# Optimization experiments

Measured on AMD Instinct MI355X. Metric: run time of the kernel, lower is better.

## Reference

```python
import jax, jax.numpy as jnp
import numpy as np

NCLASS = 21  # num_classes from init
EPS = 1e-6


def setup_inputs() -> dict:
    key = jax.random.key(0)
    k1, k2 = jax.random.split(key)
    feats = jax.random.normal(k1, (8, 256, 64, 64), dtype=jnp.float32)
    masks = jax.random.randint(k2, (8, 256, 256), 0, NCLASS, dtype=jnp.int32)
    return {"feats": feats, "masks": masks}


def reference(feats, masks):
    # feats: [B, C, h, w] float; masks: [B, H, W] int labels
    B, C, _, _ = feats.shape
    H, W = masks.shape[-2:]
    # F.interpolate(..., mode='bilinear', align_corners=False) == half-pixel bilinear resize
    f = jax.image.resize(feats, (B, C, H, W), method="bilinear")  # [B,C,H,W]
    f_flat = f.reshape(B, C, H * W)  # [B,C,P]

    # labels > nclass (e.g. 255 ignore) are clamped to the dump bucket `nclass`;
    # pixels with label == nclass are excluded (one_hot drops out-of-range rows).
    lbl = jnp.where(masks > NCLASS, NCLASS, masks).reshape(B, H * W)  # [B,P]
    onehot = jax.nn.one_hot(lbl, NCLASS, dtype=f.dtype)  # [B,P,K], dump bucket -> all zeros

    # segment-reduce: per-image per-class feature sums and pixel counts
    sums = jnp.einsum("bcp,bpk->bkc", f_flat, onehot)  # [B,K,C]
    counts = onehot.sum(axis=1)  # [B,K]
    per_img = sums / (counts[..., None] + EPS)  # [B,K,C]; absent classes -> ~0, matching torch loop skip
    prototypes = per_img.mean(axis=0)  # [K,C] (sum over batch / b)
    return prototypes
```

## Files before the change

### kernel.cpp

```cpp
#include <hip/hip_runtime.h>

#define NK 21
#define NC 256
#define NSRC 64
#define NOUT 256
#define NB 8
#define EPS 1e-6f

__device__ __forceinline__ void lds_fadd(float* p, float v) {
  __hip_atomic_fetch_add(p, v, __ATOMIC_RELAXED, __HIP_MEMORY_SCOPE_WORKGROUP);
}

__device__ __forceinline__ void glb_fadd(float* p, float v) {
  __hip_atomic_fetch_add(p, v, __ATOMIC_RELAXED, __HIP_MEMORY_SCOPE_AGENT);
}

__global__ __launch_bounds__(256, 4)
void proto_main(const float* __restrict__ feats,
                const int* __restrict__ masks,
                float* __restrict__ psum,
                float* __restrict__ pcnt) {
  __shared__ __align__(16) float Wl[NK * 32];
  __shared__ int hist[NK];

  const int tid = threadIdx.x;
  const int r0 = blockIdx.x;
  const int b = blockIdx.y;
  const int z = blockIdx.z;

  const float4* fbase = (const float4*)(
      feats + ((size_t)(b * NC + tid) << 12) + (size_t)r0 * 64 + 32 * z);
  const float4 f0 = fbase[0], f1 = fbase[1], f2 = fbase[2], f3 = fbase[3];
  const float4 f4 = fbase[4], f5 = fbase[5], f6 = fbase[6], f7 = fbase[7];

  for (int i = tid; i < NK * 32; i += 256) Wl[i] = 0.f;
  if (tid < NK) hist[tid] = 0;
  __syncthreads();

  int ylo = 4 * r0 - 2; if (ylo < 0) ylo = 0;
  int yhi = 4 * r0 + 5; if (yhi > NOUT - 1) yhi = NOUT - 1;
  const int xlo = z ? 126 : 0;
  const int npix = (yhi - ylo + 1) * 130;
  const int own_lo = 4 * r0;

  for (int i = tid; i < npix; i += 256) {
    const int x = xlo + i % 130;
    const int y = ylo + i / 130;
    const int lbl = masks[((size_t)b * NOUT + y) * NOUT + x];
    if ((unsigned)lbl < NK) {
      const int ry = y >> 2, py = y & 3;
      const int j0y = (py < 2) ? ry - 1 : ry;
      const float fy = (py == 0) ? 0.625f : (py == 1) ? 0.875f
                     : (py == 2) ? 0.125f : 0.375f;
      const int rx = x >> 2, px = x & 3;
      const int j0x = (px < 2) ? rx - 1 : rx;
      const float fx = (px == 0) ? 0.625f : (px == 1) ? 0.875f
                     : (px == 2) ? 0.125f : 0.375f;

      const int cx0 = (j0x < 0) ? 0 : j0x;
      const int cx1 = (j0x + 1 > NSRC - 1) ? NSRC - 1 : j0x + 1;
      const float wx0 = 1.f - fx, wx1 = fx;
      const int ry0 = (j0y < 0) ? 0 : j0y;
      const int ry1 = (j0y + 1 > NSRC - 1) ? NSRC - 1 : j0y + 1;
      const float wy0 = 1.f - fy, wy1 = fy;

      float* Wk = &Wl[lbl * 32];
      if (ry0 == r0) {
        if ((cx0 >> 5) == z) lds_fadd(&Wk[cx0 & 31], wy0 * wx0);
        if ((cx1 >> 5) == z) lds_fadd(&Wk[cx1 & 31], wy0 * wx1);
      }
      if (ry1 == r0) {
        if ((cx0 >> 5) == z) lds_fadd(&Wk[cx0 & 31], wy1 * wx0);
        if ((cx1 >> 5) == z) lds_fadd(&Wk[cx1 & 31], wy1 * wx1);
      }
      if (y >= own_lo && y < own_lo + 4 && (x >> 7) == z)
        atomicAdd(&hist[lbl], 1);
    }
  }
  __syncthreads();

  float acc[NK];
#pragma unroll
  for (int k = 0; k < NK; ++k) acc[k] = 0.f;

  const float4* wb = (const float4*)Wl;
#pragma unroll
  for (int k = 0; k < NK; ++k) {
    const float4 w0 = wb[k * 8 + 0], w1 = wb[k * 8 + 1];
    const float4 w2 = wb[k * 8 + 2], w3 = wb[k * 8 + 3];
    float a = acc[k];
    a = fmaf(f0.x, w0.x, a); a = fmaf(f0.y, w0.y, a);
    a = fmaf(f0.z, w0.z, a); a = fmaf(f0.w, w0.w, a);
    a = fmaf(f1.x, w1.x, a); a = fmaf(f1.y, w1.y, a);
    a = fmaf(f1.z, w1.z, a); a = fmaf(f1.w, w1.w, a);
    a = fmaf(f2.x, w2.x, a); a = fmaf(f2.y, w2.y, a);
    a = fmaf(f2.z, w2.z, a); a = fmaf(f2.w, w2.w, a);
    a = fmaf(f3.x, w3.x, a); a = fmaf(f3.y, w3.y, a);
    a = fmaf(f3.z, w3.z, a); a = fmaf(f3.w, w3.w, a);
    acc[k] = a;
  }
#pragma unroll
  for (int k = 0; k < NK; ++k) {
    const float4 w4 = wb[k * 8 + 4], w5 = wb[k * 8 + 5];
    const float4 w6 = wb[k * 8 + 6], w7 = wb[k * 8 + 7];
    float a = acc[k];
    a = fmaf(f4.x, w4.x, a); a = fmaf(f4.y, w4.y, a);
    a = fmaf(f4.z, w4.z, a); a = fmaf(f4.w, w4.w, a);
    a = fmaf(f5.x, w5.x, a); a = fmaf(f5.y, w5.y, a);
    a = fmaf(f5.z, w5.z, a); a = fmaf(f5.w, w5.w, a);
    a = fmaf(f6.x, w6.x, a); a = fmaf(f6.y, w6.y, a);
    a = fmaf(f6.z, w6.z, a); a = fmaf(f6.w, w6.w, a);
    a = fmaf(f7.x, w7.x, a); a = fmaf(f7.y, w7.y, a);
    a = fmaf(f7.z, w7.z, a); a = fmaf(f7.w, w7.w, a);
    acc[k] = a;
  }

#pragma unroll
  for (int k = 0; k < NK; ++k)
    glb_fadd(&psum[((size_t)b * NK + k) * NC + tid], acc[k]);
  if (tid < NK) glb_fadd(&pcnt[(size_t)b * NK + tid], (float)hist[tid]);
}

__global__ __launch_bounds__(256)
void proto_final(const float* __restrict__ psum,
                 const float* __restrict__ pcnt,
                 float* __restrict__ out) {
  const int k = blockIdx.x;
  const int c = threadIdx.x;
  float a = 0.f;
#pragma unroll
  for (int b = 0; b < NB; ++b)
    a += psum[((size_t)b * NK + k) * NC + c] / (pcnt[(size_t)b * NK + k] + EPS);
  out[(size_t)k * NC + c] = a * 0.125f;
}

extern "C" void kernel_launch(void* const* d_in, const int* in_sizes, int n_in,
                              void* d_out, int out_size, void* d_ws, size_t ws_size,
                              hipStream_t stream) {
  const float* feats = (const float*)d_in[0];
  const int* masks = (const int*)d_in[1];
  float* out = (float*)d_out;

  float* psum = (float*)d_ws;
  float* pcnt = psum + (size_t)NB * NK * NC;
  const size_t zbytes = ((size_t)NB * NK * NC + (size_t)NB * NK) * 4;

  hipMemsetAsync(d_ws, 0, zbytes, stream);
  proto_main<<<dim3(64, NB, 2), 256, 0, stream>>>(feats, masks, psum, pcnt);
  proto_final<<<dim3(NK), 256, 0, stream>>>(psum, pcnt, out);
}
```

Baseline: 110.6 us.

## Replace global atomics with per-slice partial buffers and drop memset

New measurement: 102.9 us. 1.08x faster.

```diff
diff --git a/kernel.cpp b/kernel.cpp
--- a/kernel.cpp
+++ b/kernel.cpp
@@ -5,21 +5,22 @@
 #define NSRC 64
 #define NOUT 256
 #define NB 8
+#define NSL 128
 #define EPS 1e-6f
 
 __device__ __forceinline__ void lds_fadd(float* p, float v) {
   __hip_atomic_fetch_add(p, v, __ATOMIC_RELAXED, __HIP_MEMORY_SCOPE_WORKGROUP);
 }
-
 __device__ __forceinline__ void glb_fadd(float* p, float v) {
   __hip_atomic_fetch_add(p, v, __ATOMIC_RELAXED, __HIP_MEMORY_SCOPE_AGENT);
 }
 
-__global__ __launch_bounds__(256, 4)
+__global__ __launch_bounds__(128, 4)
 void proto_main(const float* __restrict__ feats,
                 const int* __restrict__ masks,
                 float* __restrict__ psum,
-                float* __restrict__ pcnt) {
+                float* __restrict__ pcnt,
+                float* __restrict__ out) {
   __shared__ __align__(16) float Wl[NK * 32];
   __shared__ int hist[NK];
 
@@ -28,12 +29,19 @@
   const int b = blockIdx.y;
   const int z = blockIdx.z;
 
-  const float4* fbase = (const float4*)(
+  const float4* fb0 = (const float4*)(
       feats + ((size_t)(b * NC + tid) << 12) + (size_t)r0 * 64 + 32 * z);
-  const float4 f0 = fbase[0], f1 = fbase[1], f2 = fbase[2], f3 = fbase[3];
-  const float4 f4 = fbase[4], f5 = fbase[5], f6 = fbase[6], f7 = fbase[7];
+  const float4* fb1 = (const float4*)(
+      feats + ((size_t)(b * NC + tid + 128) << 12) + (size_t)r0 * 64 + 32 * z);
+  const float4 f0 = fb0[0], f1 = fb0[1], f2 = fb0[2], f3 = fb0[3];
+  const float4 f4 = fb0[4], f5 = fb0[5], f6 = fb0[6], f7 = fb0[7];
+  const float4 g0 = fb1[0], g1 = fb1[1], g2 = fb1[2], g3 = fb1[3];
+  const float4 g4 = fb1[4], g5 = fb1[5], g6 = fb1[6], g7 = fb1[7];
 
-  for (int i = tid; i < NK * 32; i += 256) Wl[i] = 0.f;
+  if (r0 == 0 && b == 0 && z == 0)
+    for (int i = tid; i < NK * NC; i += 128) out[i] = 0.f;
+
+  for (int i = tid; i < NK * 32; i += 128) Wl[i] = 0.f;
   if (tid < NK) hist[tid] = 0;
   __syncthreads();
 
@@ -43,7 +51,7 @@
   const int npix = (yhi - ylo + 1) * 130;
   const int own_lo = 4 * r0;
 
-  for (int i = tid; i < npix; i += 256) {
+  for (int i = tid; i < npix; i += 128) {
     const int x = xlo + i % 130;
     const int y = ylo + i / 130;
     const int lbl = masks[((size_t)b * NOUT + y) * NOUT + x];
@@ -79,46 +87,52 @@
   }
   __syncthreads();
 
-  float acc[NK];
-#pragma unroll
-  for (int k = 0; k < NK; ++k) acc[k] = 0.f;
-
+  const int sl = r0 * 2 + z;
+  float* dst = psum + ((size_t)(b * NSL + sl) * NK) * NC;
   const float4* wb = (const float4*)Wl;
 #pragma unroll
   for (int k = 0; k < NK; ++k) {
     const float4 w0 = wb[k * 8 + 0], w1 = wb[k * 8 + 1];
     const float4 w2 = wb[k * 8 + 2], w3 = wb[k * 8 + 3];
-    float a = acc[k];
-    a = fmaf(f0.x, w0.x, a); a = fmaf(f0.y, w0.y, a);
-    a = fmaf(f0.z, w0.z, a); a = fmaf(f0.w, w0.w, a);
-    a = fmaf(f1.x, w1.x, a); a = fmaf(f1.y, w1.y, a);
-    a = fmaf(f1.z, w1.z, a); a = fmaf(f1.w, w1.w, a);
-    a = fmaf(f2.x, w2.x, a); a = fmaf(f2.y, w2.y, a);
-    a = fmaf(f2.z, w2.z, a); a = fmaf(f2.w, w2.w, a);
-    a = fmaf(f3.x, w3.x, a); a = fmaf(f3.y, w3.y, a);
-    a = fmaf(f3.z, w3.z, a); a = fmaf(f3.w, w3.w, a);
-    acc[k] = a;
-  }
-#pragma unroll
-  for (int k = 0; k < NK; ++k) {
     const float4 w4 = wb[k * 8 + 4], w5 = wb[k * 8 + 5];
     const float4 w6 = wb[k * 8 + 6], w7 = wb[k * 8 + 7];
-    float a = acc[k];
-    a = fmaf(f4.x, w4.x, a); a = fmaf(f4.y, w4.y, a);
-    a = fmaf(f4.z, w4.z, a); a = fmaf(f4.w, w4.w, a);
-    a = fmaf(f5.x, w5.x, a); a = fmaf(f5.y, w5.y, a);
-    a = fmaf(f5.z, w5.z, a); a = fmaf(f5.w, w5.w, a);
-    a = fmaf(f6.x, w6.x, a); a = fmaf(f6.y, w6.y, a);
-    a = fmaf(f6.z, w6.z, a); a = fmaf(f6.w, w6.w, a);
-    a = fmaf(f7.x, w7.x, a); a = fmaf(f7.y, w7.y, a);
-    a = fmaf(f7.z, w7.z, a); a = fmaf(f7.w, w7.w, a);
-    acc[k] = a;
+    float a0 = 0.f, a1 = 0.f;
+    a0 = fmaf(f0.x, w0.x, a0); a0 = fmaf(f0.y, w0.y, a0);
+    a0 = fmaf(f0.z, w0.z, a0); a0 = fmaf(f0.w, w0.w, a0);
+    a0 = fmaf(f1.x, w1.x, a0); a0 = fmaf(f1.y, w1.y, a0);
+    a0 = fmaf(f1.z, w1.z, a0); a0 = fmaf(f1.w, w1.w, a0);
+    a0 = fmaf(f2.x, w2.x, a0); a0 = fmaf(f2.y, w2.y, a0);
+    a0 = fmaf(f2.z, w2.z, a0); a0 = fmaf(f2.w, w2.w, a0);
+    a0 = fmaf(f3.x, w3.x, a0); a0 = fmaf(f3.y, w3.y, a0);
+    a0 = fmaf(f3.z, w3.z, a0); a0 = fmaf(f3.w, w3.w, a0);
+    a0 = fmaf(f4.x, w4.x, a0); a0 = fmaf(f4.y, w4.y, a0);
+    a0 = fmaf(f4.z, w4.z, a0); a0 = fmaf(f4.w, w4.w, a0);
+    a0 = fmaf(f5.x, w5.x, a0); a0 = fmaf(f5.y, w5.y, a0);
+    a0 = fmaf(f5.z, w5.z, a0); a0 = fmaf(f5.w, w5.w, a0);
+    a0 = fmaf(f6.x, w6.x, a0); a0 = fmaf(f6.y, w6.y, a0);
+    a0 = fmaf(f6.z, w6.z, a0); a0 = fmaf(f6.w, w6.w, a0);
+    a0 = fmaf(f7.x, w7.x, a0); a0 = fmaf(f7.y, w7.y, a0);
+    a0 = fmaf(f7.z, w7.z, a0); a0 = fmaf(f7.w, w7.w, a0);
+    a1 = fmaf(g0.x, w0.x, a1); a1 = fmaf(g0.y, w0.y, a1);
+    a1 = fmaf(g0.z, w0.z, a1); a1 = fmaf(g0.w, w0.w, a1);
+    a1 = fmaf(g1.x, w1.x, a1); a1 = fmaf(g1.y, w1.y, a1);
+    a1 = fmaf(g1.z, w1.z, a1); a1 = fmaf(g1.w, w1.w, a1);
+    a1 = fmaf(g2.x, w2.x, a1); a1 = fmaf(g2.y, w2.y, a1);
+    a1 = fmaf(g2.z, w2.z, a1); a1 = fmaf(g2.w, w2.w, a1);
+    a1 = fmaf(g3.x, w3.x, a1); a1 = fmaf(g3.y, w3.y, a1);
+    a1 = fmaf(g3.z, w3.z, a1); a1 = fmaf(g3.w, w3.w, a1);
+    a1 = fmaf(g4.x, w4.x, a1); a1 = fmaf(g4.y, w4.y, a1);
+    a1 = fmaf(g4.z, w4.z, a1); a1 = fmaf(g4.w, w4.w, a1);
+    a1 = fmaf(g5.x, w5.x, a1); a1 = fmaf(g5.y, w5.y, a1);
+    a1 = fmaf(g5.z, w5.z, a1); a1 = fmaf(g5.w, w5.w, a1);
+    a1 = fmaf(g6.x, w6.x, a1); a1 = fmaf(g6.y, w6.y, a1);
+    a1 = fmaf(g6.z, w6.z, a1); a1 = fmaf(g6.w, w6.w, a1);
+    a1 = fmaf(g7.x, w7.x, a1); a1 = fmaf(g7.y, w7.y, a1);
+    a1 = fmaf(g7.z, w7.z, a1); a1 = fmaf(g7.w, w7.w, a1);
+    dst[k * NC + tid] = a0;
+    dst[k * NC + tid + 128] = a1;
   }
-
-#pragma unroll
-  for (int k = 0; k < NK; ++k)
-    glb_fadd(&psum[((size_t)b * NK + k) * NC + tid], acc[k]);
-  if (tid < NK) glb_fadd(&pcnt[(size_t)b * NK + tid], (float)hist[tid]);
+  if (tid < NK) pcnt[(size_t)(b * NSL + sl) * NK + tid] = (float)hist[tid];
 }
 
 __global__ __launch_bounds__(256)
@@ -126,12 +140,22 @@
                  const float* __restrict__ pcnt,
                  float* __restrict__ out) {
   const int k = blockIdx.x;
+  const int b = blockIdx.y;
   const int c = threadIdx.x;
-  float a = 0.f;
+  float s0 = 0.f, s1 = 0.f, s2 = 0.f, s3 = 0.f, cnt = 0.f;
 #pragma unroll
-  for (int b = 0; b < NB; ++b)
-    a += psum[((size_t)b * NK + k) * NC + c] / (pcnt[(size_t)b * NK + k] + EPS);
-  out[(size_t)k * NC + c] = a * 0.125f;
+  for (int sl = 0; sl < NSL; sl += 4) {
+    s0 += psum[((size_t)(b * NSL + sl + 0) * NK + k) * NC + c];
+    s1 += psum[((size_t)(b * NSL + sl + 1) * NK + k) * NC + c];
+    s2 += psum[((size_t)(b * NSL + sl + 2) * NK + k) * NC + c];
+    s3 += psum[((size_t)(b * NSL + sl + 3) * NK + k) * NC + c];
+    cnt += pcnt[(size_t)(b * NSL + sl + 0) * NK + k];
+    cnt += pcnt[(size_t)(b * NSL + sl + 1) * NK + k];
+    cnt += pcnt[(size_t)(b * NSL + sl + 2) * NK + k];
+    cnt += pcnt[(size_t)(b * NSL + sl + 3) * NK + k];
+  }
+  const float v = ((s0 + s1) + (s2 + s3)) / (cnt + EPS) * 0.125f;
+  glb_fadd(&out[k * NC + c], v);
 }
 
 extern "C" void kernel_launch(void* const* d_in, const int* in_sizes, int n_in,
@@ -142,10 +166,8 @@
   float* out = (float*)d_out;
 
   float* psum = (float*)d_ws;
-  float* pcnt = psum + (size_t)NB * NK * NC;
-  const size_t zbytes = ((size_t)NB * NK * NC + (size_t)NB * NK) * 4;
+  float* pcnt = psum + (size_t)NB * NSL * NK * NC;
 
-  hipMemsetAsync(d_ws, 0, zbytes, stream);
-  proto_main<<<dim3(64, NB, 2), 256, 0, stream>>>(feats, masks, psum, pcnt);
-  proto_final<<<dim3(NK), 256, 0, stream>>>(psum, pcnt, out);
+  proto_main<<<dim3(64, NB, 2), 128, 0, stream>>>(feats, masks, psum, pcnt, out);
+  proto_final<<<dim3(NK, NB), 256, 0, stream>>>(psum, pcnt, out);
 }
```

## Replace global atomics with per-slice partial buffers and drop memset

Applied to the files above, without the earlier changes.

Result: faster. 102.3 us (-7.6%).

```diff
diff --git a/kernel.cpp b/kernel.cpp
--- a/kernel.cpp
+++ b/kernel.cpp
@@ -5,12 +5,12 @@
 #define NSRC 64
 #define NOUT 256
 #define NB 8
+#define NSL 128
 #define EPS 1e-6f
 
 __device__ __forceinline__ void lds_fadd(float* p, float v) {
   __hip_atomic_fetch_add(p, v, __ATOMIC_RELAXED, __HIP_MEMORY_SCOPE_WORKGROUP);
 }
-
 __device__ __forceinline__ void glb_fadd(float* p, float v) {
   __hip_atomic_fetch_add(p, v, __ATOMIC_RELAXED, __HIP_MEMORY_SCOPE_AGENT);
 }
@@ -19,7 +19,8 @@
 void proto_main(const float* __restrict__ feats,
                 const int* __restrict__ masks,
                 float* __restrict__ psum,
-                float* __restrict__ pcnt) {
+                float* __restrict__ pcnt,
+                float* __restrict__ out) {
   __shared__ __align__(16) float Wl[NK * 32];
   __shared__ int hist[NK];
 
@@ -28,14 +29,16 @@
   const int b = blockIdx.y;
   const int z = blockIdx.z;
 
+  for (int i = tid; i < NK * 32; i += 256) Wl[i] = 0.f;
+  if (tid < NK) hist[tid] = 0;
+  if (r0 == 0 && b == 0 && z == 0)
+    for (int i = tid; i < NK * NC; i += 256) out[i] = 0.f;
+  __syncthreads();
+
   const float4* fbase = (const float4*)(
       feats + ((size_t)(b * NC + tid) << 12) + (size_t)r0 * 64 + 32 * z);
   const float4 f0 = fbase[0], f1 = fbase[1], f2 = fbase[2], f3 = fbase[3];
   const float4 f4 = fbase[4], f5 = fbase[5], f6 = fbase[6], f7 = fbase[7];
-
-  for (int i = tid; i < NK * 32; i += 256) Wl[i] = 0.f;
-  if (tid < NK) hist[tid] = 0;
-  __syncthreads();
 
   int ylo = 4 * r0 - 2; if (ylo < 0) ylo = 0;
   int yhi = 4 * r0 + 5; if (yhi > NOUT - 1) yhi = NOUT - 1;
@@ -115,10 +118,11 @@
     acc[k] = a;
   }
 
+  const int sl = r0 * 2 + z;
+  float* dst = psum + ((size_t)(b * NSL + sl) * NK) * NC + tid;
 #pragma unroll
-  for (int k = 0; k < NK; ++k)
-    glb_fadd(&psum[((size_t)b * NK + k) * NC + tid], acc[k]);
-  if (tid < NK) glb_fadd(&pcnt[(size_t)b * NK + tid], (float)hist[tid]);
+  for (int k = 0; k < NK; ++k) dst[k * NC] = acc[k];
+  if (tid < NK) pcnt[(size_t)(b * NSL + sl) * NK + tid] = (float)hist[tid];
 }
 
 __global__ __launch_bounds__(256)
@@ -126,12 +130,22 @@
                  const float* __restrict__ pcnt,
                  float* __restrict__ out) {
   const int k = blockIdx.x;
+  const int b = blockIdx.y;
   const int c = threadIdx.x;
-  float a = 0.f;
+  float s0 = 0.f, s1 = 0.f, s2 = 0.f, s3 = 0.f, cnt = 0.f;
 #pragma unroll
-  for (int b = 0; b < NB; ++b)
-    a += psum[((size_t)b * NK + k) * NC + c] / (pcnt[(size_t)b * NK + k] + EPS);
-  out[(size_t)k * NC + c] = a * 0.125f;
+  for (int sl = 0; sl < NSL; sl += 4) {
+    s0 += psum[((size_t)(b * NSL + sl + 0) * NK + k) * NC + c];
+    s1 += psum[((size_t)(b * NSL + sl + 1) * NK + k) * NC + c];
+    s2 += psum[((size_t)(b * NSL + sl + 2) * NK + k) * NC + c];
+    s3 += psum[((size_t)(b * NSL + sl + 3) * NK + k) * NC + c];
+    cnt += pcnt[(size_t)(b * NSL + sl + 0) * NK + k];
+    cnt += pcnt[(size_t)(b * NSL + sl + 1) * NK + k];
+    cnt += pcnt[(size_t)(b * NSL + sl + 2) * NK + k];
+    cnt += pcnt[(size_t)(b * NSL + sl + 3) * NK + k];
+  }
+  const float v = ((s0 + s1) + (s2 + s3)) / (cnt + EPS) * 0.125f;
+  glb_fadd(&out[k * NC + c], v);
 }
 
 extern "C" void kernel_launch(void* const* d_in, const int* in_sizes, int n_in,
@@ -142,10 +156,8 @@
   float* out = (float*)d_out;
 
   float* psum = (float*)d_ws;
-  float* pcnt = psum + (size_t)NB * NK * NC;
-  const size_t zbytes = ((size_t)NB * NK * NC + (size_t)NB * NK) * 4;
+  float* pcnt = psum + (size_t)NB * NSL * NK * NC;
 
-  hipMemsetAsync(d_ws, 0, zbytes, stream);
-  proto_main<<<dim3(64, NB, 2), 256, 0, stream>>>(feats, masks, psum, pcnt);
-  proto_final<<<dim3(NK), 256, 0, stream>>>(psum, pcnt, out);
+  proto_main<<<dim3(64, NB, 2), 256, 0, stream>>>(feats, masks, psum, pcnt, out);
+  proto_final<<<dim3(NK, NB), 256, 0, stream>>>(psum, pcnt, out);
 }
```
